# Kernel optimization log

Hardware: AMD Instinct MI355X
Metric: run time of the kernel (lower is better)

Reference implementation:

```python
import jax, jax.numpy as jnp
import numpy as np

VOCAB = 50000
DIM = 768


def setup_inputs() -> dict:
    key = jax.random.key(0)
    k1, k2, k3, k4 = jax.random.split(key, 4)
    token = jax.random.randint(k1, (32, 512), 0, VOCAB, dtype=jnp.int64)
    need_mapper = jax.random.randint(k2, (VOCAB,), 0, 2, dtype=jnp.int32)
    bert_embedding = jax.random.normal(k3, (VOCAB, DIM), dtype=jnp.float32)
    mapper_w = jax.random.normal(k4, (DIM, DIM), dtype=jnp.float32) * (1.0 / np.sqrt(DIM))
    mapper_b = jnp.zeros((DIM,), dtype=jnp.float32)
    return {
        "token": token,
        "need_mapper": need_mapper,
        "bert_embedding": bert_embedding,
        "mapper_w": mapper_w,
        "mapper_b": mapper_b,
    }


def reference(token, need_mapper, bert_embedding, mapper_w, mapper_b):
    # Gather: [B, S, D] -- irregular access into the embedding table.
    vecs = bert_embedding[token]
    # Conditional mapper (vectorized over all tokens; selected by per-id mask).
    mapped = jnp.einsum("bsd,de->bse", vecs, mapper_w) + mapper_b
    need = need_mapper[token].astype(bool)  # [B, S]
    return jnp.where(need[..., None], mapped, vecs)
```

## Files before the change

kernel.cpp:

```cpp
#include <hip/hip_runtime.h>
#include <hip/hip_bf16.h>
#include <stdint.h>
#include <stddef.h>

#define DIM 768

typedef short short8 __attribute__((ext_vector_type(8)));
typedef float f32x4 __attribute__((ext_vector_type(4)));

__device__ inline unsigned short f2bf_rne(float f) {
    union { float f; unsigned u; } x; x.f = f;
    unsigned r = x.u + 0x7fffu + ((x.u >> 16) & 1u);
    return (unsigned short)(r >> 16);
}

__device__ inline void gload_lds16(const void* g, void* l) {
    __builtin_amdgcn_global_load_lds((const __attribute__((address_space(1))) void*)g,
                                     (__attribute__((address_space(3))) void*)l, 16, 0, 0);
}

__global__ __launch_bounds__(256) void emb_gather_kernel(
    const int* __restrict__ token,
    const int* __restrict__ need_mapper,
    const float* __restrict__ emb,
    float* __restrict__ out,
    unsigned short* __restrict__ Abf,
    int* __restrict__ flags,
    int ntok)
{
    int idx = blockIdx.x * 256 + threadIdx.x;
    int trow = idx / 192;
    if (trow >= ntok) return;
    int d4 = idx - trow * 192;
    int tok = token[trow];
    int need = need_mapper[tok];
    const float4* src = (const float4*)(emb + (size_t)tok * DIM) + d4;
    float4 v = *src;
    ushort4 h;
    h.x = f2bf_rne(v.x); h.y = f2bf_rne(v.y);
    h.z = f2bf_rne(v.z); h.w = f2bf_rne(v.w);
    *((ushort4*)(Abf + (size_t)trow * DIM) + d4) = h;
    if (!need) {
        *((float4*)(out + (size_t)trow * DIM) + d4) = v;
    }
    if (d4 == 0) flags[trow] = need;
}

__global__ __launch_bounds__(256) void convw_kernel(
    const float* __restrict__ w, unsigned short* __restrict__ Bt)
{
    int idx = blockIdx.x * 256 + threadIdx.x;
    if (idx >= DIM * DIM) return;
    int k = idx / DIM;
    int n = idx - k * DIM;
    Bt[(size_t)n * DIM + k] = f2bf_rne(w[idx]);
}

__global__ __launch_bounds__(256) void gemm_map_kernel(
    const unsigned short* __restrict__ A,
    const unsigned short* __restrict__ Bt,
    const float* __restrict__ bias,
    const int* __restrict__ flags,
    float* __restrict__ out)
{
    __shared__ unsigned short As[128 * 32];
    __shared__ unsigned short Bs[128 * 32];

    const int tid  = threadIdx.x;
    const int wave = tid >> 6;
    const int lane = tid & 63;
    const int quad = lane >> 4;
    const int l15  = lane & 15;
    const int wm   = wave >> 1;
    const int wn   = wave & 1;
    const int tile_m = blockIdx.x;
    const int tile_n = blockIdx.y;

    const int srow = tid >> 2;
    const int scol = (tid & 3) * 8;

    const unsigned short* Ag = A  + (size_t)(tile_m * 128 + srow) * DIM + scol;
    const unsigned short* Bg = Bt + (size_t)(tile_n * 128 + srow) * DIM + scol;

    unsigned short* AsW = As + wave * 512;
    unsigned short* BsW = Bs + wave * 512;

    f32x4 acc[4][4] = {};

    for (int kk = 0; kk < DIM; kk += 32) {
        __syncthreads();
        gload_lds16(Ag + kk,            AsW);
        gload_lds16(Ag + kk + 64 * DIM, AsW + 2048);
        gload_lds16(Bg + kk,            BsW);
        gload_lds16(Bg + kk + 64 * DIM, BsW + 2048);
        __syncthreads();

        short8 af[4], bf[4];
#pragma unroll
        for (int i = 0; i < 4; ++i)
            af[i] = *(const short8*)(As + (wm * 64 + i * 16 + l15) * 32 + quad * 8);
#pragma unroll
        for (int j = 0; j < 4; ++j)
            bf[j] = *(const short8*)(Bs + (wn * 64 + j * 16 + l15) * 32 + quad * 8);
#pragma unroll
        for (int i = 0; i < 4; ++i)
#pragma unroll
            for (int j = 0; j < 4; ++j)
                acc[i][j] = __builtin_amdgcn_mfma_f32_16x16x32_bf16(af[i], bf[j], acc[i][j], 0, 0, 0);
    }

    const int colg = tile_n * 128 + wn * 64 + l15;
    float bv[4];
#pragma unroll
    for (int j = 0; j < 4; ++j) bv[j] = bias[colg + j * 16];

    const int row0 = tile_m * 128 + wm * 64 + quad * 4;
#pragma unroll
    for (int i = 0; i < 4; ++i) {
#pragma unroll
        for (int r = 0; r < 4; ++r) {
            int gm = row0 + i * 16 + r;
            if (flags[gm] != 0) {
                float* orow = out + (size_t)gm * DIM + colg;
#pragma unroll
                for (int j = 0; j < 4; ++j)
                    orow[j * 16] = acc[i][j][r] + bv[j];
            }
        }
    }
}

extern "C" void kernel_launch(void* const* d_in, const int* in_sizes, int n_in,
                              void* d_out, int out_size, void* d_ws, size_t ws_size,
                              hipStream_t stream)
{
    const int*   token       = (const int*)d_in[0];
    const int*   need_mapper = (const int*)d_in[1];
    const float* emb         = (const float*)d_in[2];
    const float* w           = (const float*)d_in[3];
    const float* bias        = (const float*)d_in[4];
    float* out = (float*)d_out;

    const int ntok = in_sizes[0];

    unsigned short* Abf = (unsigned short*)d_ws;
    unsigned short* Bt  = (unsigned short*)((char*)d_ws + (size_t)ntok * DIM * 2);
    int* flags          = (int*)((char*)d_ws + (size_t)ntok * DIM * 2 + (size_t)DIM * DIM * 2);

    int gthreads = ntok * (DIM / 4);
    emb_gather_kernel<<<dim3((gthreads + 255) / 256), dim3(256), 0, stream>>>(
        token, need_mapper, emb, out, Abf, flags, ntok);
    convw_kernel<<<dim3((DIM * DIM + 255) / 256), dim3(256), 0, stream>>>(w, Bt);
    dim3 grid(ntok / 128, DIM / 128);
    gemm_map_kernel<<<grid, dim3(256), 0, stream>>>(Abf, Bt, bias, flags, out);
}
```

Baseline: 254.3 us.

## Fuse embedding gather into GEMM and tile the weight transpose through LDS

The separate gather kernel is removed. The GEMM now looks up token ids and need flags itself, loads fp32 embedding rows straight into LDS with an XOR swizzle, converts them to bf16 at fragment load, and copies unmapped rows from the table in the epilogue. The weight transpose now goes through a padded 64x64 LDS tile so that reads and writes are coalesced. This removes the bf16 A-matrix round trip through global memory and one kernel launch. In exchange, each of the six N-tiles re-reads the fp32 rows (twice the LDS and global bytes for A), and rounding becomes round-half-up instead of round-to-nearest-even.

```diff
diff --git a/kernel.cpp b/kernel.cpp
--- a/kernel.cpp
+++ b/kernel.cpp
@@ -19,52 +19,39 @@
                                      (__attribute__((address_space(3))) void*)l, 16, 0, 0);
 }
 
-__global__ __launch_bounds__(256) void emb_gather_kernel(
+__global__ __launch_bounds__(256) void convw_kernel(
+    const float* __restrict__ w, unsigned short* __restrict__ Bt)
+{
+    __shared__ unsigned short t[64][65];
+    const int k0 = blockIdx.x * 64, n0 = blockIdx.y * 64;
+    const int tid = threadIdx.x;
+#pragma unroll
+    for (int p = 0; p < 16; ++p) {
+        int e = p * 256 + tid;
+        int r = e >> 6, c = e & 63;
+        t[c][r] = f2bf_rne(w[(size_t)(k0 + r) * DIM + n0 + c]);
+    }
+    __syncthreads();
+#pragma unroll
+    for (int p = 0; p < 16; ++p) {
+        int e = p * 256 + tid;
+        int r = e >> 6, c = e & 63;
+        Bt[(size_t)(n0 + r) * DIM + k0 + c] = t[r][c];
+    }
+}
+
+__global__ __launch_bounds__(256) void fused_gemm_kernel(
     const int* __restrict__ token,
     const int* __restrict__ need_mapper,
     const float* __restrict__ emb,
-    float* __restrict__ out,
-    unsigned short* __restrict__ Abf,
-    int* __restrict__ flags,
-    int ntok)
-{
-    int idx = blockIdx.x * 256 + threadIdx.x;
-    int trow = idx / 192;
-    if (trow >= ntok) return;
-    int d4 = idx - trow * 192;
-    int tok = token[trow];
-    int need = need_mapper[tok];
-    const float4* src = (const float4*)(emb + (size_t)tok * DIM) + d4;
-    float4 v = *src;
-    ushort4 h;
-    h.x = f2bf_rne(v.x); h.y = f2bf_rne(v.y);
-    h.z = f2bf_rne(v.z); h.w = f2bf_rne(v.w);
-    *((ushort4*)(Abf + (size_t)trow * DIM) + d4) = h;
-    if (!need) {
-        *((float4*)(out + (size_t)trow * DIM) + d4) = v;
-    }
-    if (d4 == 0) flags[trow] = need;
-}
-
-__global__ __launch_bounds__(256) void convw_kernel(
-    const float* __restrict__ w, unsigned short* __restrict__ Bt)
-{
-    int idx = blockIdx.x * 256 + threadIdx.x;
-    if (idx >= DIM * DIM) return;
-    int k = idx / DIM;
-    int n = idx - k * DIM;
-    Bt[(size_t)n * DIM + k] = f2bf_rne(w[idx]);
-}
-
-__global__ __launch_bounds__(256) void gemm_map_kernel(
-    const unsigned short* __restrict__ A,
     const unsigned short* __restrict__ Bt,
     const float* __restrict__ bias,
-    const int* __restrict__ flags,
     float* __restrict__ out)
 {
-    __shared__ unsigned short As[128 * 32];
+    __shared__ float As[128 * 32];
     __shared__ unsigned short Bs[128 * 32];
+    __shared__ int tok_s[128];
+    __shared__ int flag_s[128];
 
     const int tid  = threadIdx.x;
     const int wave = tid >> 6;
@@ -76,29 +63,58 @@
     const int tile_m = blockIdx.x;
     const int tile_n = blockIdx.y;
 
-    const int srow = tid >> 2;
-    const int scol = (tid & 3) * 8;
+    if (tid < 128) {
+        int t = token[tile_m * 128 + tid];
+        tok_s[tid]  = t;
+        flag_s[tid] = need_mapper[t];
+    }
+    __syncthreads();
 
-    const unsigned short* Ag = A  + (size_t)(tile_m * 128 + srow) * DIM + scol;
-    const unsigned short* Bg = Bt + (size_t)(tile_n * 128 + srow) * DIM + scol;
-
-    unsigned short* AsW = As + wave * 512;
-    unsigned short* BsW = Bs + wave * 512;
+    const int r8 = tid >> 3;
+    const int c8 = tid & 7;
+    const float* pA[4];
+#pragma unroll
+    for (int j = 0; j < 4; ++j) {
+        int r = j * 32 + r8;
+        pA[j] = emb + (size_t)tok_s[r] * DIM + ((c8 ^ (r & 7)) << 2);
+    }
+    float* lA0 = As + (wave * 8) * 32;
+    const unsigned short* pB = Bt + (size_t)(tile_n * 128 + (tid >> 2)) * DIM + (tid & 3) * 8;
+    unsigned short* lB = Bs + wave * 512;
 
     f32x4 acc[4][4] = {};
 
     for (int kk = 0; kk < DIM; kk += 32) {
         __syncthreads();
-        gload_lds16(Ag + kk,            AsW);
-        gload_lds16(Ag + kk + 64 * DIM, AsW + 2048);
-        gload_lds16(Bg + kk,            BsW);
-        gload_lds16(Bg + kk + 64 * DIM, BsW + 2048);
+#pragma unroll
+        for (int j = 0; j < 4; ++j)
+            gload_lds16(pA[j] + kk, lA0 + j * 32 * 32);
+        gload_lds16(pB + kk,                   lB);
+        gload_lds16(pB + kk + (size_t)64 * DIM, lB + 2048);
         __syncthreads();
 
         short8 af[4], bf[4];
 #pragma unroll
-        for (int i = 0; i < 4; ++i)
-            af[i] = *(const short8*)(As + (wm * 64 + i * 16 + l15) * 32 + quad * 8);
+        for (int i = 0; i < 4; ++i) {
+            const int m = wm * 64 + i * 16 + l15;
+            const float* row = As + (m << 5);
+            f32x4 a0 = *(const f32x4*)(row + ((((quad << 1)    ) ^ (m & 7)) << 2));
+            f32x4 a1 = *(const f32x4*)(row + ((((quad << 1) + 1) ^ (m & 7)) << 2));
+            unsigned u0 = __float_as_uint(a0[0]) + 0x8000u;
+            unsigned u1 = __float_as_uint(a0[1]) + 0x8000u;
+            unsigned u2 = __float_as_uint(a0[2]) + 0x8000u;
+            unsigned u3 = __float_as_uint(a0[3]) + 0x8000u;
+            unsigned u4 = __float_as_uint(a1[0]) + 0x8000u;
+            unsigned u5 = __float_as_uint(a1[1]) + 0x8000u;
+            unsigned u6 = __float_as_uint(a1[2]) + 0x8000u;
+            unsigned u7 = __float_as_uint(a1[3]) + 0x8000u;
+            union { int i4[4]; short8 s; } pk;
+            pk.i4[0] = __builtin_amdgcn_perm(u1, u0, 0x07060302);
+            pk.i4[1] = __builtin_amdgcn_perm(u3, u2, 0x07060302);
+            pk.i4[2] = __builtin_amdgcn_perm(u5, u4, 0x07060302);
+            pk.i4[3] = __builtin_amdgcn_perm(u7, u6, 0x07060302);
+            af[i] = pk.s;
+        }
 #pragma unroll
         for (int j = 0; j < 4; ++j)
             bf[j] = *(const short8*)(Bs + (wn * 64 + j * 16 + l15) * 32 + quad * 8);
@@ -114,17 +130,22 @@
 #pragma unroll
     for (int j = 0; j < 4; ++j) bv[j] = bias[colg + j * 16];
 
-    const int row0 = tile_m * 128 + wm * 64 + quad * 4;
 #pragma unroll
     for (int i = 0; i < 4; ++i) {
 #pragma unroll
         for (int r = 0; r < 4; ++r) {
-            int gm = row0 + i * 16 + r;
-            if (flags[gm] != 0) {
-                float* orow = out + (size_t)gm * DIM + colg;
+            const int lrow = wm * 64 + i * 16 + quad * 4 + r;
+            const int gm   = tile_m * 128 + lrow;
+            float* orow = out + (size_t)gm * DIM + colg;
+            if (flag_s[lrow]) {
 #pragma unroll
                 for (int j = 0; j < 4; ++j)
                     orow[j * 16] = acc[i][j][r] + bv[j];
+            } else {
+                const float* erow = emb + (size_t)tok_s[lrow] * DIM + colg;
+#pragma unroll
+                for (int j = 0; j < 4; ++j)
+                    orow[j * 16] = erow[j * 16];
             }
         }
     }
@@ -143,14 +164,9 @@
 
     const int ntok = in_sizes[0];
 
-    unsigned short* Abf = (unsigned short*)d_ws;
-    unsigned short* Bt  = (unsigned short*)((char*)d_ws + (size_t)ntok * DIM * 2);
-    int* flags          = (int*)((char*)d_ws + (size_t)ntok * DIM * 2 + (size_t)DIM * DIM * 2);
+    unsigned short* Bt = (unsigned short*)d_ws;
 
-    int gthreads = ntok * (DIM / 4);
-    emb_gather_kernel<<<dim3((gthreads + 255) / 256), dim3(256), 0, stream>>>(
-        token, need_mapper, emb, out, Abf, flags, ntok);
-    convw_kernel<<<dim3((DIM * DIM + 255) / 256), dim3(256), 0, stream>>>(w, Bt);
-    dim3 grid(ntok / 128, DIM / 128);
-    gemm_map_kernel<<<grid, dim3(256), 0, stream>>>(Abf, Bt, bias, flags, out);
+    convw_kernel<<<dim3(DIM / 64, DIM / 64), dim3(256), 0, stream>>>(w, Bt);
+    fused_gemm_kernel<<<dim3(ntok / 128, DIM / 128), dim3(256), 0, stream>>>(
+        token, need_mapper, emb, Bt, bias, out);
 }
```

Result: faster. 242.8 us (-4.5%).

## Fuse gather and weight transpose into one prep kernel; swizzle GEMM LDS

Applied to the files above, without the earlier changes.

Merges the embedding gather/bf16 conversion and the weight transpose into a single launch. The transpose now goes through a padded LDS tile so both reads and writes are coalesced. The gather handles 8 floats per thread, with truncate-plus-round packing done by perm instructions. The GEMM gets an XOR swizzle on its LDS chunk layout to cut bank conflicts, and its grid is reordered so blocks sharing an A tile are scheduled together. The bf16 rounding changes from round-to-nearest-even to round-half-up, which slightly changes numerics.

```diff
diff --git a/kernel.cpp b/kernel.cpp
--- a/kernel.cpp
+++ b/kernel.cpp
@@ -19,44 +19,67 @@
                                      (__attribute__((address_space(3))) void*)l, 16, 0, 0);
 }
 
-__global__ __launch_bounds__(256) void emb_gather_kernel(
+#define NWBLK 144
+__global__ __launch_bounds__(256) void prep_kernel(
     const int* __restrict__ token,
     const int* __restrict__ need_mapper,
     const float* __restrict__ emb,
+    const float* __restrict__ w,
     float* __restrict__ out,
     unsigned short* __restrict__ Abf,
-    int* __restrict__ flags,
-    int ntok)
+    unsigned short* __restrict__ Bt,
+    int* __restrict__ flags)
 {
-    int idx = blockIdx.x * 256 + threadIdx.x;
-    int trow = idx / 192;
-    if (trow >= ntok) return;
-    int d4 = idx - trow * 192;
-    int tok = token[trow];
+    const int tid = threadIdx.x;
+    if (blockIdx.x < NWBLK) {
+        __shared__ unsigned short t[64][65];
+        const int k0 = (blockIdx.x / 12) * 64, n0 = (blockIdx.x % 12) * 64;
+#pragma unroll
+        for (int p = 0; p < 16; ++p) {
+            int e = p * 256 + tid;
+            int r = e >> 6, c = e & 63;
+            t[c][r] = f2bf_rne(w[(size_t)(k0 + r) * DIM + n0 + c]);
+        }
+        __syncthreads();
+#pragma unroll
+        for (int p = 0; p < 16; ++p) {
+            int e = p * 256 + tid;
+            int r = e >> 6, c = e & 63;
+            Bt[(size_t)(n0 + r) * DIM + k0 + c] = t[r][c];
+        }
+        return;
+    }
+    int e = (blockIdx.x - NWBLK) * 256 + tid;
+    int r = e / 96;
+    int q = e - r * 96;
+    int tok = token[r];
     int need = need_mapper[tok];
-    const float4* src = (const float4*)(emb + (size_t)tok * DIM) + d4;
-    float4 v = *src;
-    ushort4 h;
-    h.x = f2bf_rne(v.x); h.y = f2bf_rne(v.y);
-    h.z = f2bf_rne(v.z); h.w = f2bf_rne(v.w);
-    *((ushort4*)(Abf + (size_t)trow * DIM) + d4) = h;
+    const float* src = emb + (size_t)tok * DIM + q * 8;
+    float4 v0 = *(const float4*)src;
+    float4 v1 = *(const float4*)(src + 4);
+    unsigned u0 = __float_as_uint(v0.x) + 0x8000u;
+    unsigned u1 = __float_as_uint(v0.y) + 0x8000u;
+    unsigned u2 = __float_as_uint(v0.z) + 0x8000u;
+    unsigned u3 = __float_as_uint(v0.w) + 0x8000u;
+    unsigned u4 = __float_as_uint(v1.x) + 0x8000u;
+    unsigned u5 = __float_as_uint(v1.y) + 0x8000u;
+    unsigned u6 = __float_as_uint(v1.z) + 0x8000u;
+    unsigned u7 = __float_as_uint(v1.w) + 0x8000u;
+    union { int i4[4]; short8 s; } pk;
+    pk.i4[0] = __builtin_amdgcn_perm(u1, u0, 0x07060302);
+    pk.i4[1] = __builtin_amdgcn_perm(u3, u2, 0x07060302);
+    pk.i4[2] = __builtin_amdgcn_perm(u5, u4, 0x07060302);
+    pk.i4[3] = __builtin_amdgcn_perm(u7, u6, 0x07060302);
+    *(short8*)(Abf + (size_t)r * DIM + q * 8) = pk.s;
     if (!need) {
-        *((float4*)(out + (size_t)trow * DIM) + d4) = v;
+        float* dst = out + (size_t)r * DIM + q * 8;
+        *(float4*)dst = v0;
+        *(float4*)(dst + 4) = v1;
     }
-    if (d4 == 0) flags[trow] = need;
+    if (q == 0) flags[r] = need;
 }
 
-__global__ __launch_bounds__(256) void convw_kernel(
-    const float* __restrict__ w, unsigned short* __restrict__ Bt)
-{
-    int idx = blockIdx.x * 256 + threadIdx.x;
-    if (idx >= DIM * DIM) return;
-    int k = idx / DIM;
-    int n = idx - k * DIM;
-    Bt[(size_t)n * DIM + k] = f2bf_rne(w[idx]);
-}
-
-__global__ __launch_bounds__(256) void gemm_map_kernel(
+__global__ __launch_bounds__(256) void gemm_kernel(
     const unsigned short* __restrict__ A,
     const unsigned short* __restrict__ Bt,
     const float* __restrict__ bias,
@@ -73,17 +96,18 @@
     const int l15  = lane & 15;
     const int wm   = wave >> 1;
     const int wn   = wave & 1;
-    const int tile_m = blockIdx.x;
-    const int tile_n = blockIdx.y;
+    const int tile_n = blockIdx.x;
+    const int tile_m = blockIdx.y;
 
     const int srow = tid >> 2;
-    const int scol = (tid & 3) * 8;
-
-    const unsigned short* Ag = A  + (size_t)(tile_m * 128 + srow) * DIM + scol;
-    const unsigned short* Bg = Bt + (size_t)(tile_n * 128 + srow) * DIM + scol;
+    const int schk = (tid & 3) ^ ((srow >> 1) & 3);
+    const unsigned short* Ag = A  + (size_t)(tile_m * 128 + srow) * DIM + schk * 8;
+    const unsigned short* Bg = Bt + (size_t)(tile_n * 128 + srow) * DIM + schk * 8;
 
     unsigned short* AsW = As + wave * 512;
     unsigned short* BsW = Bs + wave * 512;
+
+    const int slot = quad ^ ((l15 >> 1) & 3);
 
     f32x4 acc[4][4] = {};
 
@@ -98,10 +122,10 @@
         short8 af[4], bf[4];
 #pragma unroll
         for (int i = 0; i < 4; ++i)
-            af[i] = *(const short8*)(As + (wm * 64 + i * 16 + l15) * 32 + quad * 8);
+            af[i] = *(const short8*)(As + (wm * 64 + i * 16 + l15) * 32 + slot * 8);
 #pragma unroll
         for (int j = 0; j < 4; ++j)
-            bf[j] = *(const short8*)(Bs + (wn * 64 + j * 16 + l15) * 32 + quad * 8);
+            bf[j] = *(const short8*)(Bs + (wn * 64 + j * 16 + l15) * 32 + slot * 8);
 #pragma unroll
         for (int i = 0; i < 4; ++i)
 #pragma unroll
@@ -145,12 +169,11 @@
 
     unsigned short* Abf = (unsigned short*)d_ws;
     unsigned short* Bt  = (unsigned short*)((char*)d_ws + (size_t)ntok * DIM * 2);
-    int* flags          = (int*)((char*)d_ws + (size_t)ntok * DIM * 2 + (size_t)DIM * DIM * 2);
+    int* flags = (int*)((char*)d_ws + (size_t)ntok * DIM * 2 + (size_t)DIM * DIM * 2);
 
-    int gthreads = ntok * (DIM / 4);
-    emb_gather_kernel<<<dim3((gthreads + 255) / 256), dim3(256), 0, stream>>>(
-        token, need_mapper, emb, out, Abf, flags, ntok);
-    convw_kernel<<<dim3((DIM * DIM + 255) / 256), dim3(256), 0, stream>>>(w, Bt);
-    dim3 grid(ntok / 128, DIM / 128);
-    gemm_map_kernel<<<grid, dim3(256), 0, stream>>>(Abf, Bt, bias, flags, out);
+    int gblocks = NWBLK + (ntok * (DIM / 8)) / 256;
+    prep_kernel<<<dim3(gblocks), dim3(256), 0, stream>>>(
+        token, need_mapper, emb, w, out, Abf, Bt, flags);
+    gemm_kernel<<<dim3(DIM / 128, ntok / 128), dim3(256), 0, stream>>>(
+        Abf, Bt, bias, flags, out);
 }
```

After: 252.5 us. About the same (-0.7%).
